# Optimization experiments

Measured on AMD Instinct MI355X. Metric: run time of the kernel, lower is better.

The kernel has to match this reference:

```python
import jax, jax.numpy as jnp
import numpy as np

B, A, L, D, IN = 4096, 11, 8, 256, 4
HID = 64  # mlp_dim in MS_HGNN modules
LINE = 64  # line_embedding output dim


def setup_inputs() -> dict:
    key = jax.random.key(0)
    ks = jax.random.split(key, 17)
    s = 0.02
    f = jnp.float32
    return {
        "inputs": jax.random.normal(ks[0], (B * A, L, IN), f),
        "W_in": jax.random.normal(ks[1], (IN, D), f) * s,
        "b_in": jnp.zeros((D,), f),
        "W_pos": jax.random.normal(ks[2], (2 * D, D), f) * s,
        "b_pos": jnp.zeros((D,), f),
        "W_fc2": jax.random.normal(ks[3], (L * D, D), f) * s,
        "b_fc2": jnp.zeros((D,), f),
        "W_fc3": jax.random.normal(ks[4], (D + A, D), f) * s,
        "b_fc3": jnp.zeros((D,), f),
        "Wh1": jax.random.normal(ks[5], (D, HID), f) * s,
        "We1": jax.random.normal(ks[6], (2 * HID, HID), f) * s,
        "Wn1": jax.random.normal(ks[7], (HID, D), f) * s,
        "Wh2": jax.random.normal(ks[8], (D, HID), f) * s,
        "We2": jax.random.normal(ks[9], (2 * HID, HID), f) * s,
        "Wn2": jax.random.normal(ks[10], (HID, D), f) * s,
        "W_line": jax.random.normal(ks[11], (D, LINE), f) * s,
        "batch_size": B,
        "agent_num": A,
    }


def _nmp(xf, Wh, We, Wn, w=None):
    # one round of neural message passing over the (hyper)graph of agents
    h = jax.nn.relu(xf @ Wh)  # [B, A, HID]
    b, a, hd = h.shape
    hi = jnp.broadcast_to(h[:, :, None, :], (b, a, a, hd))
    hj = jnp.broadcast_to(h[:, None, :, :], (b, a, a, hd))
    e = jax.nn.relu(jnp.concatenate([hi, hj], -1) @ We)  # [B, A, A, HID]
    if w is None:
        agg = e.mean(axis=2)
    else:
        agg = (w[..., None] * e).sum(axis=2) / (w.sum(axis=2)[..., None] + 1e-6)
    return agg @ Wn  # [B, A, D]


def reference(inputs, W_in, b_in, W_pos, b_pos, W_fc2, b_fc2, W_fc3, b_fc3,
              Wh1, We1, Wn1, Wh2, We2, Wn2, W_line, batch_size, agent_num):
    d = W_in.shape[1]
    length = inputs.shape[1]
    # input_fc
    tf_in = inputs @ W_in + b_in  # [B*A, L, D]
    # positional encoding (sin/cos interleaved), concat + fc (dropout in eval)
    pos = jnp.arange(length, dtype=tf_in.dtype)[:, None]
    div = jnp.exp(jnp.arange(0, d, 2, dtype=tf_in.dtype) * (-np.log(10000.0) / d))
    ang = pos * div  # [L, D/2]
    pe = jnp.stack([jnp.sin(ang), jnp.cos(ang)], -1).reshape(length, d)
    x = jnp.concatenate([tf_in, jnp.broadcast_to(pe, tf_in.shape)], -1) @ W_pos + b_pos
    # flatten time, input_fc2
    x = x.reshape(batch_size, agent_num, length * d)
    ftraj = x @ W_fc2 + b_fc2  # [B, A, D]
    # add_category (identity one-hot per agent) + input_fc3
    eye = jnp.broadcast_to(jnp.eye(agent_num, dtype=ftraj.dtype),
                           (batch_size, agent_num, agent_num))
    ftraj = jnp.concatenate([ftraj, eye], -1) @ W_fc3 + b_fc3
    # cosine-similarity correlation + per-scene adaptive thresholding
    q = ftraj / jnp.linalg.norm(ftraj, axis=2, keepdims=True)
    corr = jnp.einsum('bad,bcd->bac', q, q)
    a = corr.min(axis=(1, 2), keepdims=True)
    thr = jnp.where(a < 0.4, 0.4,
                    jnp.where((a > 0.4) & (a < 0.6), a + 0.1, a + 0.03))
    corr = jnp.where(corr < thr, jnp.zeros_like(corr), corr)
    adj = (corr > 0).astype(ftraj.dtype)  # binarized dynamic grouping mask
    # ordinary fully-connected interaction
    ftraj_inter = _nmp(ftraj, Wh1, We1, Wn1)
    # group-masked hyper interaction + line embedding
    hyp = _nmp(ftraj, Wh2, We2, Wn2, adj)
    feat_one = hyp @ W_line  # [B, A, LINE]
    out = jnp.concatenate([ftraj, ftraj_inter, feat_one], -1)
    return out.reshape(batch_size * agent_num, -1)
```

## Files before the change

### kernel.cpp

```cpp
#include <hip/hip_runtime.h>

#define TPB 256
#define TPM 192

constexpr int B_ = 4096, A_ = 11;
constexpr int R_ = B_ * A_;

constexpr int M_O     = 0;
constexpr int M2_O    = 8192;
constexpr int WC_O    = 16384;
constexpr int XB_O    = 17408;
constexpr int CB_O    = 19456;
constexpr int B2_O    = 19712;
constexpr int WN2L_O  = 22528;
constexpr int MH1_O   = 26624;
constexpr int BH1_O   = 28672;
constexpr int MH2_O   = 29376;
constexpr int BH2_O   = 31424;
constexpr int WFA1_O  = 32768;
constexpr int WFA2_O  = 49152;
constexpr int BEYE1_O = 65536;
constexpr int BEYE2_O = 66240;
constexpr int BB1_O   = 66944;
constexpr int BB2_O   = 67008;
constexpr int AG1_O   = 67584;
constexpr int SZ_RH   = R_ * 64;
constexpr int AG2_O   = AG1_O + SZ_RH;


__global__ __launch_bounds__(TPB) void k_preA(const float* __restrict__ Win,
                                              const float* __restrict__ bin,
                                              const float* __restrict__ Wpos,
                                              const float* __restrict__ bpos,
                                              const float* __restrict__ Wn2,
                                              const float* __restrict__ Wline,
                                              const float* __restrict__ Wfc3,
                                              const float* __restrict__ bfc3,
                                              const float* __restrict__ Wh1,
                                              const float* __restrict__ Wh2,
                                              float* __restrict__ ws) {
    __shared__ float red[8 * 33];
    const int t = threadIdx.x, o8 = t & 31, ks = t >> 5;
    const int bx = blockIdx.x;
    float p = 0.f;
    float base_add = 0.f;
    int out_idx = -1;
    if (bx < 64) {
        int o = bx * 32 + o8, l = o >> 8, j = o & 255;
        const float c0 = -logf(10000.f) / 256.f;
        for (int d = ks * 64; d < ks * 64 + 64; ++d) {
            float a;
            if (d < 256) a = bin[d];
            else {
                int dd = d - 256;
                float freq = expf((float)(dd & ~1) * c0);
                float ang = (float)l * freq;
                a = (dd & 1) ? cosf(ang) : sinf(ang);
            }
            p += a * Wpos[d * 256 + j];
        }
        out_idx = XB_O + o; base_add = bpos[j];
    } else if (bx < 192) {
        int o = (bx - 64) * 32 + o8, k = o >> 6, c = o & 63;
        #pragma unroll 8
        for (int d = ks * 32; d < ks * 32 + 32; ++d) p += Wn2[k * 256 + d] * Wline[d * 64 + c];
        out_idx = WN2L_O + o;
    } else if (bx < 704) {
        int o = (bx - 192) * 32 + o8, e = o >> 6, c = o & 63;
        #pragma unroll 8
        for (int d = ks * 32; d < ks * 32 + 32; ++d) p += Wfc3[e * 256 + d] * Wh1[d * 64 + c];
        out_idx = WFA1_O + o;
    } else if (bx < 1216) {
        int o = (bx - 704) * 32 + o8, e = o >> 6, c = o & 63;
        #pragma unroll 8
        for (int d = ks * 32; d < ks * 32 + 32; ++d) p += Wfc3[e * 256 + d] * Wh2[d * 64 + c];
        out_idx = WFA2_O + o;
    } else if (bx < 1238) {
        int o = (bx - 1216) * 32 + o8, a = o >> 6, c = o & 63;
        #pragma unroll 8
        for (int d = ks * 32; d < ks * 32 + 32; ++d) p += Wfc3[(256 + a) * 256 + d] * Wh1[d * 64 + c];
        out_idx = BEYE1_O + o;
    } else if (bx < 1260) {
        int o = (bx - 1238) * 32 + o8, a = o >> 6, c = o & 63;
        #pragma unroll 8
        for (int d = ks * 32; d < ks * 32 + 32; ++d) p += Wfc3[(256 + a) * 256 + d] * Wh2[d * 64 + c];
        out_idx = BEYE2_O + o;
    } else if (bx < 1262) {
        int c = (bx - 1260) * 32 + o8;
        #pragma unroll 8
        for (int d = ks * 32; d < ks * 32 + 32; ++d) p += bfc3[d] * Wh1[d * 64 + c];
        out_idx = BB1_O + c;
    } else if (bx < 1264) {
        int c = (bx - 1262) * 32 + o8;
        #pragma unroll 8
        for (int d = ks * 32; d < ks * 32 + 32; ++d) p += bfc3[d] * Wh2[d * 64 + c];
        out_idx = BB2_O + c;
    } else {
        int o = (bx - 1264) * 32 + o8, i = o >> 8, j = o & 255;
        #pragma unroll 8
        for (int d = ks * 32; d < ks * 32 + 32; ++d) p += Win[i * 256 + d] * Wpos[d * 256 + j];
        out_idx = WC_O + o;
    }
    red[ks * 33 + o8] = p;
    __shared__ float baseS[32];
    if (ks == 0) baseS[o8] = base_add;
    __syncthreads();
    if (t < 32) {
        float s = baseS[t];
        #pragma unroll
        for (int m = 0; m < 8; ++m) s += red[m * 33 + t];
        ws[out_idx - o8 + t] = s;
    }
}

__global__ __launch_bounds__(TPB) void k_preC(const float* __restrict__ Wfc2,
                                              const float* __restrict__ bfc2,
                                              float* __restrict__ ws) {
    __shared__ float red[8 * 33];
    const int t = threadIdx.x, o8 = t & 31, ks = t >> 5;
    const int bx = blockIdx.x;
    if (bx < 256) {
        int o = bx * 32 + o8, k = o >> 8, j = o & 255;
        int l = k >> 2, i = k & 3;
        const float* Ar = ws + WC_O + i * 256;
        const float* Br = Wfc2 + l * 65536 + j;
        float p = 0.f;
        #pragma unroll 8
        for (int d = ks * 32; d < ks * 32 + 32; ++d) p += Ar[d] * Br[d * 256];
        red[ks * 33 + o8] = p;
        __syncthreads();
        if (t < 32) {
            float s = 0.f;
            #pragma unroll
            for (int m = 0; m < 8; ++m) s += red[m * 33 + t];
            ws[M_O + bx * 32 + t] = s;
        }
    } else {
        int j = (bx - 256) * 32 + o8;
        const float* Ar = ws + XB_O;
        float p = 0.f;
        #pragma unroll 4
        for (int dk = ks * 256; dk < ks * 256 + 256; ++dk) p += Ar[dk] * Wfc2[dk * 256 + j];
        red[ks * 33 + o8] = p;
        __syncthreads();
        if (t < 32) {
            int jj = (bx - 256) * 32 + t;
            float s = bfc2[jj];
            #pragma unroll
            for (int m = 0; m < 8; ++m) s += red[m * 33 + t];
            ws[CB_O + jj] = s;
        }
    }
}

__global__ __launch_bounds__(TPB) void k_preD(const float* __restrict__ Wfc3,
                                              const float* __restrict__ bfc3,
                                              float* __restrict__ ws) {
    __shared__ float red[8 * 33];
    const int t = threadIdx.x, o8 = t & 31, ks = t >> 5;
    const int bx = blockIdx.x;
    float p = 0.f;
    int out_base = -1;
    int oo32 = 0;
    if (bx < 256) {
        int o = bx * 32 + o8, k = o >> 8, j = o & 255;
        const float* Ar = ws + M_O + k * 256;
        #pragma unroll 8
        for (int d = ks * 32; d < ks * 32 + 32; ++d) p += Ar[d] * Wfc3[d * 256 + j];
        out_base = M2_O; oo32 = bx * 32;
    } else if (bx < 344) {
        int o = (bx - 256) * 32 + o8, j = o & 255;
        const float* Ar = ws + CB_O;
        #pragma unroll 8
        for (int d = ks * 32; d < ks * 32 + 32; ++d) p += Ar[d] * Wfc3[d * 256 + j];
        out_base = B2_O; oo32 = (bx - 256) * 32;
    } else if (bx < 408) {
        int o = (bx - 344) * 32 + o8, k = o >> 6, c = o & 63;
        const float* Ar = ws + M_O + k * 256;
        const float* Br = ws + WFA1_O;
        #pragma unroll 8
        for (int d = ks * 32; d < ks * 32 + 32; ++d) p += Ar[d] * Br[d * 64 + c];
        out_base = MH1_O; oo32 = (bx - 344) * 32;
    } else if (bx < 472) {
        int o = (bx - 408) * 32 + o8, k = o >> 6, c = o & 63;
        const float* Ar = ws + M_O + k * 256;
        const float* Br = ws + WFA2_O;
        #pragma unroll 8
        for (int d = ks * 32; d < ks * 32 + 32; ++d) p += Ar[d] * Br[d * 64 + c];
        out_base = MH2_O; oo32 = (bx - 408) * 32;
    } else if (bx < 494) {
        int o = (bx - 472) * 32 + o8, c = o & 63;
        const float* Ar = ws + CB_O;
        const float* Br = ws + WFA1_O;
        #pragma unroll 8
        for (int d = ks * 32; d < ks * 32 + 32; ++d) p += Ar[d] * Br[d * 64 + c];
        out_base = BH1_O; oo32 = (bx - 472) * 32;
    } else {
        int o = (bx - 494) * 32 + o8, c = o & 63;
        const float* Ar = ws + CB_O;
        const float* Br = ws + WFA2_O;
        #pragma unroll 8
        for (int d = ks * 32; d < ks * 32 + 32; ++d) p += Ar[d] * Br[d * 64 + c];
        out_base = BH2_O; oo32 = (bx - 494) * 32;
    }
    red[ks * 33 + o8] = p;
    __syncthreads();
    if (t < 32) {
        int oo = oo32 + t;
        float s;
        if (out_base == B2_O) {
            int aa = oo >> 8, jj = oo & 255;
            s = bfc3[jj] + Wfc3[(256 + aa) * 256 + jj];
        } else if (out_base == BH1_O) {
            int aa = oo >> 6, cc = oo & 63;
            s = ws[BB1_O + cc] + ws[BEYE1_O + aa * 64 + cc];
        } else if (out_base == BH2_O) {
            int aa = oo >> 6, cc = oo & 63;
            s = ws[BB2_O + cc] + ws[BEYE2_O + aa * 64 + cc];
        } else s = 0.f;
        #pragma unroll
        for (int m = 0; m < 8; ++m) s += red[m * 33 + t];
        ws[out_base + oo] = s;
    }
}


__global__ __launch_bounds__(TPM) void k_main(const float* __restrict__ in,
                                              const float* __restrict__ We1g,
                                              const float* __restrict__ We2g,
                                              float* ws,
                                              float* out) {
    __shared__ float inS[22 * 36];
    __shared__ float buf[22 * 68];
    __shared__ float Bs[2048];
    __shared__ float dcS[242];
    __shared__ float thrS[2];
    const int t = threadIdx.x;
    const int rg = t >> 4, cg = t & 15;
    const int r0 = rg * 2, c0 = cg * 4;
    const int rowBlk = blockIdx.x * 22;
    const bool act = rg < 11;

    float4 pf0, pf1, pf2;
    auto pfLoad = [&](const float4* lo, const float4* hi) {
        pf0 = lo[t];
        pf1 = (t < 64) ? lo[t + 192] : hi[t - 64];
        if (t < 128) pf2 = hi[t + 128];
    };
    auto pfStore = [&]() {
        float4* d = (float4*)Bs;
        d[t] = pf0; d[t + 192] = pf1;
        if (t < 128) d[t + 384] = pf2;
    };

    pfLoad((const float4*)(ws + M2_O), (const float4*)(ws + M2_O) + 256);
    for (int o = t; o < 176; o += TPM) {
        int row = o >> 3, c4 = o & 7;
        *(float4*)&inS[row * 36 + c4 * 4] =
            *(const float4*)&in[(size_t)(rowBlk + row) * 32 + c4 * 4];
    }
    __syncthreads();

    float acc[2][16];
    #pragma unroll
    for (int r = 0; r < 2; ++r)
        #pragma unroll
        for (int c = 0; c < 16; ++c) acc[r][c] = 0.f;
    for (int kh = 0; kh < 4; ++kh) {
        pfStore();
        if (kh < 3) pfLoad((const float4*)(ws + M2_O) + (kh + 1) * 512,
                           (const float4*)(ws + M2_O) + (kh + 1) * 512 + 256);
        else        pfLoad((const float4*)(ws + MH1_O), (const float4*)(ws + MH1_O) + 256);
        __syncthreads();
        if (act) {
            #pragma unroll
            for (int kq = 0; kq < 2; ++kq) {
                float av[2][4];
                #pragma unroll
                for (int r = 0; r < 2; ++r) {
                    float4 a4 = *(const float4*)&inS[(r0 + r) * 36 + kh * 8 + kq * 4];
                    av[r][0] = a4.x; av[r][1] = a4.y; av[r][2] = a4.z; av[r][3] = a4.w;
                }
                #pragma unroll
                for (int kk = 0; kk < 4; ++kk) {
                    float4 b[4];
                    #pragma unroll
                    for (int j = 0; j < 4; ++j)
                        b[j] = *(const float4*)&Bs[(kq * 4 + kk) * 256 + c0 + j * 64];
                    #pragma unroll
                    for (int r = 0; r < 2; ++r) {
                        float a = av[r][kk];
                        #pragma unroll
                        for (int j = 0; j < 4; ++j) {
                            acc[r][j * 4 + 0] += a * b[j].x;
                            acc[r][j * 4 + 1] += a * b[j].y;
                            acc[r][j * 4 + 2] += a * b[j].z;
                            acc[r][j * 4 + 3] += a * b[j].w;
                        }
                    }
                }
            }
        }
        __syncthreads();
    }
    if (act) {
        #pragma unroll
        for (int r = 0; r < 2; ++r) {
            int row = r0 + r, il = row % 11;
            size_t ob = (size_t)(rowBlk + row) * 576;
            #pragma unroll
            for (int j = 0; j < 4; ++j) {
                float4 b2 = *(const float4*)&ws[B2_O + il * 256 + c0 + j * 64];
                acc[r][j * 4 + 0] += b2.x; acc[r][j * 4 + 1] += b2.y;
                acc[r][j * 4 + 2] += b2.z; acc[r][j * 4 + 3] += b2.w;
                *(float4*)&out[ob + c0 + j * 64] =
                    make_float4(acc[r][j * 4 + 0], acc[r][j * 4 + 1],
                                acc[r][j * 4 + 2], acc[r][j * 4 + 3]);
            }
        }
    }

    bool has0 = false;
    int s0_ = 0, i0_ = 0, j0_ = 0;
    if (t < 132) {
        has0 = true; s0_ = t / 66; int p = t % 66; int i = 0;
        while (p >= 11 - i) { p -= 11 - i; ++i; }
        i0_ = i; j0_ = i + p;
    }
    float dacc0 = 0.f;
    #pragma unroll
    for (int sl = 0; sl < 4; ++sl) {
        if (act) {
            #pragma unroll
            for (int r = 0; r < 2; ++r)
                *(float4*)&buf[(r0 + r) * 68 + c0] =
                    make_float4(acc[r][sl * 4 + 0], acc[r][sl * 4 + 1],
                                acc[r][sl * 4 + 2], acc[r][sl * 4 + 3]);
        }
        __syncthreads();
        if (has0) {
            const float* ra = &buf[(s0_ * 11 + i0_) * 68];
            const float* rb = &buf[(s0_ * 11 + j0_) * 68];
            #pragma unroll
            for (int c = 0; c < 16; ++c) {
                float4 a = *(const float4*)&ra[c * 4];
                float4 b = *(const float4*)&rb[c * 4];
                dacc0 += a.x * b.x + a.y * b.y + a.z * b.z + a.w * b.w;
            }
        }
        __syncthreads();
    }
    if (has0) { dcS[s0_ * 121 + i0_ * 11 + j0_] = dacc0;
                dcS[s0_ * 121 + j0_ * 11 + i0_] = dacc0; }
    __syncthreads();

    {
        float cc0, cc1 = 0.f;
        {
            int idx = t; int si = idx / 121, p = idx % 121, i = p / 11, j = p % 11;
            cc0 = dcS[idx] * rsqrtf(dcS[si * 121 + i * 12] * dcS[si * 121 + j * 12]);
        }
        if (t + TPM < 242) {
            int idx = t + TPM; int si = idx / 121, p = idx % 121, i = p / 11, j = p % 11;
            cc1 = dcS[idx] * rsqrtf(dcS[si * 121 + i * 12] * dcS[si * 121 + j * 12]);
        }
        __syncthreads();
        dcS[t] = cc0;
        if (t + TPM < 242) dcS[t + TPM] = cc1;
    }
    __syncthreads();
    if (t < 2) {
        float mn = 3.0e38f;
        for (int p = 0; p < 121; ++p) mn = fminf(mn, dcS[t * 121 + p]);
        thrS[t] = (mn < 0.4f) ? 0.4f : ((mn > 0.4f && mn < 0.6f) ? mn + 0.1f : mn + 0.03f);
    }
    __syncthreads();

    for (int st = 0; st < 2; ++st) {
        const float* bh = ws + (st ? BH2_O : BH1_O);
        const float* We = st ? We2g : We1g;
        pfStore();
        pfLoad((const float4*)(We), (const float4*)(We + 4096));
        __syncthreads();
        float hh[2][4];
        #pragma unroll
        for (int r = 0; r < 2; ++r)
            #pragma unroll
            for (int c = 0; c < 4; ++c) hh[r][c] = 0.f;
        if (act) {
            #pragma unroll
            for (int kq = 0; kq < 8; ++kq) {
                float av[2][4];
                #pragma unroll
                for (int r = 0; r < 2; ++r) {
                    float4 a4 = *(const float4*)&inS[(r0 + r) * 36 + kq * 4];
                    av[r][0] = a4.x; av[r][1] = a4.y; av[r][2] = a4.z; av[r][3] = a4.w;
                }
                #pragma unroll
                for (int kk = 0; kk < 4; ++kk) {
                    float4 b = *(const float4*)&Bs[(kq * 4 + kk) * 64 + c0];
                    #pragma unroll
                    for (int r = 0; r < 2; ++r) {
                        float a = av[r][kk];
                        hh[r][0] += a * b.x; hh[r][1] += a * b.y;
                        hh[r][2] += a * b.z; hh[r][3] += a * b.w;
                    }
                }
            }
            #pragma unroll
            for (int r = 0; r < 2; ++r) {
                int il = (r0 + r) % 11;
                float4 b = *(const float4*)&bh[il * 64 + c0];
                *(float4*)&buf[(r0 + r) * 68 + c0] =
                    make_float4(fmaxf(hh[r][0] + b.x, 0.f), fmaxf(hh[r][1] + b.y, 0.f),
                                fmaxf(hh[r][2] + b.z, 0.f), fmaxf(hh[r][3] + b.w, 0.f));
            }
        }
        __syncthreads();
        float uu[2][4], vv[2][4];
        #pragma unroll
        for (int r = 0; r < 2; ++r)
            #pragma unroll
            for (int c = 0; c < 4; ++c) { uu[r][c] = 0.f; vv[r][c] = 0.f; }
        for (int kh = 0; kh < 4; ++kh) {
            pfStore();
            if (kh < 3)
                pfLoad((const float4*)(We + (kh + 1) * 1024),
                       (const float4*)(We + 4096 + (kh + 1) * 1024));
            else if (st == 0)
                pfLoad((const float4*)(ws + MH2_O), (const float4*)(ws + MH2_O) + 256);
            __syncthreads();
            if (act) {
                #pragma unroll
                for (int kq = 0; kq < 4; ++kq) {
                    float av[2][4];
                    #pragma unroll
                    for (int r = 0; r < 2; ++r) {
                        float4 a4 = *(const float4*)&buf[(r0 + r) * 68 + kh * 16 + kq * 4];
                        av[r][0] = a4.x; av[r][1] = a4.y; av[r][2] = a4.z; av[r][3] = a4.w;
                    }
                    #pragma unroll
                    for (int kk = 0; kk < 4; ++kk) {
                        float4 bu = *(const float4*)&Bs[(kq * 4 + kk) * 64 + c0];
                        float4 bv = *(const float4*)&Bs[1024 + (kq * 4 + kk) * 64 + c0];
                        #pragma unroll
                        for (int r = 0; r < 2; ++r) {
                            float a = av[r][kk];
                            uu[r][0] += a * bu.x; uu[r][1] += a * bu.y;
                            uu[r][2] += a * bu.z; uu[r][3] += a * bu.w;
                            vv[r][0] += a * bv.x; vv[r][1] += a * bv.y;
                            vv[r][2] += a * bv.z; vv[r][3] += a * bv.w;
                        }
                    }
                }
            }
            __syncthreads();
        }
        if (act) {
            #pragma unroll
            for (int r = 0; r < 2; ++r)
                *(float4*)&buf[(r0 + r) * 68 + c0] =
                    make_float4(vv[r][0], vv[r][1], vv[r][2], vv[r][3]);
        }
        __syncthreads();
        if (act) {
            float* ag = ws + (st ? AG2_O : AG1_O);
            #pragma unroll
            for (int r = 0; r < 2; ++r) {
                int row = r0 + r, s = row / 11, il = row - s * 11;
                float th = thrS[s];
                float t0 = 0.f, t1 = 0.f, t2 = 0.f, t3 = 0.f, cnt = 0.f;
                #pragma unroll
                for (int j = 0; j < 11; ++j) {
                    float4 vj = *(const float4*)&buf[(s * 11 + j) * 68 + c0];
                    if (st == 0) {
                        t0 += fmaxf(uu[r][0] + vj.x, 0.f);
                        t1 += fmaxf(uu[r][1] + vj.y, 0.f);
                        t2 += fmaxf(uu[r][2] + vj.z, 0.f);
                        t3 += fmaxf(uu[r][3] + vj.w, 0.f);
                    } else {
                        float adj = (dcS[s * 121 + il * 11 + j] >= th) ? 1.f : 0.f;
                        t0 += adj * fmaxf(uu[r][0] + vj.x, 0.f);
                        t1 += adj * fmaxf(uu[r][1] + vj.y, 0.f);
                        t2 += adj * fmaxf(uu[r][2] + vj.z, 0.f);
                        t3 += adj * fmaxf(uu[r][3] + vj.w, 0.f);
                        cnt += adj;
                    }
                }
                float inv = (st == 0) ? (1.f / 11.f) : (1.f / (cnt + 1e-6f));
                *(float4*)&ag[(size_t)(rowBlk + row) * 64 + c0] =
                    make_float4(t0 * inv, t1 * inv, t2 * inv, t3 * inv);
            }
        }
        __syncthreads();
    }
}


__global__ __launch_bounds__(TPB) void k_tail(const float* __restrict__ Wn1,
                                              const float* __restrict__ ws,
                                              float* __restrict__ out) {
    __shared__ float aS[32 * 68];
    __shared__ float Bs[2048];
    const int t = threadIdx.x;
    const int rowBase = blockIdx.x * 32;
    const int tg = t >> 4, tc = t & 15;
    const int r0 = tg * 2, c0 = tc * 4;

    {
        const float4* s1 = (const float4*)(ws + AG1_O + (size_t)rowBase * 64);
        #pragma unroll
        for (int o = t; o < 512; o += TPB) {
            int row = o >> 4, c4 = o & 15;
            *(float4*)&aS[row * 68 + c4 * 4] = s1[o];
        }
    }
    __syncthreads();

    {
        float acc[2][16];
        #pragma unroll
        for (int r = 0; r < 2; ++r)
            #pragma unroll
            for (int c = 0; c < 16; ++c) acc[r][c] = 0.f;
        for (int kh = 0; kh < 8; ++kh) {
            if (kh) __syncthreads();
            {
                const float4* src = (const float4*)(Wn1 + kh * 2048);
                float4* dst = (float4*)Bs;
                dst[t] = src[t];
                dst[t + 256] = src[t + 256];
            }
            __syncthreads();
            #pragma unroll
            for (int kq = 0; kq < 2; ++kq) {
                float av[2][4];
                #pragma unroll
                for (int r = 0; r < 2; ++r) {
                    float4 a4 = *(const float4*)&aS[(r0 + r) * 68 + kh * 8 + kq * 4];
                    av[r][0] = a4.x; av[r][1] = a4.y; av[r][2] = a4.z; av[r][3] = a4.w;
                }
                #pragma unroll
                for (int kk = 0; kk < 4; ++kk) {
                    float4 b[4];
                    #pragma unroll
                    for (int j = 0; j < 4; ++j)
                        b[j] = *(const float4*)&Bs[(kq * 4 + kk) * 256 + c0 + j * 64];
                    #pragma unroll
                    for (int r = 0; r < 2; ++r) {
                        float a = av[r][kk];
                        #pragma unroll
                        for (int j = 0; j < 4; ++j) {
                            acc[r][j * 4 + 0] += a * b[j].x;
                            acc[r][j * 4 + 1] += a * b[j].y;
                            acc[r][j * 4 + 2] += a * b[j].z;
                            acc[r][j * 4 + 3] += a * b[j].w;
                        }
                    }
                }
            }
        }
        #pragma unroll
        for (int r = 0; r < 2; ++r) {
            size_t ob = (size_t)(rowBase + r0 + r) * 576 + 256;
            #pragma unroll
            for (int j = 0; j < 4; ++j)
                *(float4*)&out[ob + c0 + j * 64] =
                    make_float4(acc[r][j * 4 + 0], acc[r][j * 4 + 1],
                                acc[r][j * 4 + 2], acc[r][j * 4 + 3]);
        }
    }

    __syncthreads();
    {
        const float4* s2 = (const float4*)(ws + AG2_O + (size_t)rowBase * 64);
        #pragma unroll
        for (int o = t; o < 512; o += TPB) {
            int row = o >> 4, c4 = o & 15;
            *(float4*)&aS[row * 68 + c4 * 4] = s2[o];
        }
    }
    {
        float fa[2][4];
        #pragma unroll
        for (int r = 0; r < 2; ++r)
            #pragma unroll
            for (int c = 0; c < 4; ++c) fa[r][c] = 0.f;
        for (int kh = 0; kh < 2; ++kh) {
            __syncthreads();
            {
                const float4* src = (const float4*)(ws + WN2L_O + kh * 2048);
                float4* dst = (float4*)Bs;
                dst[t] = src[t];
                dst[t + 256] = src[t + 256];
            }
            __syncthreads();
            #pragma unroll
            for (int kq = 0; kq < 8; ++kq) {
                float av[2][4];
                #pragma unroll
                for (int r = 0; r < 2; ++r) {
                    float4 a4 = *(const float4*)&aS[(r0 + r) * 68 + kh * 32 + kq * 4];
                    av[r][0] = a4.x; av[r][1] = a4.y; av[r][2] = a4.z; av[r][3] = a4.w;
                }
                #pragma unroll
                for (int kk = 0; kk < 4; ++kk) {
                    float4 b = *(const float4*)&Bs[(kq * 4 + kk) * 64 + c0];
                    #pragma unroll
                    for (int r = 0; r < 2; ++r) {
                        float a = av[r][kk];
                        fa[r][0] += a * b.x; fa[r][1] += a * b.y;
                        fa[r][2] += a * b.z; fa[r][3] += a * b.w;
                    }
                }
            }
        }
        #pragma unroll
        for (int r = 0; r < 2; ++r)
            *(float4*)&out[(size_t)(rowBase + r0 + r) * 576 + 512 + c0] =
                make_float4(fa[r][0], fa[r][1], fa[r][2], fa[r][3]);
    }
}

extern "C" void kernel_launch(void* const* d_in, const int* in_sizes, int n_in,
                              void* d_out, int out_size, void* d_ws, size_t ws_size,
                              hipStream_t stream) {
    (void)in_sizes; (void)n_in; (void)out_size; (void)ws_size;
    const float* in     = (const float*)d_in[0];
    const float* W_in   = (const float*)d_in[1];
    const float* b_in   = (const float*)d_in[2];
    const float* W_pos  = (const float*)d_in[3];
    const float* b_pos  = (const float*)d_in[4];
    const float* W_fc2  = (const float*)d_in[5];
    const float* b_fc2  = (const float*)d_in[6];
    const float* W_fc3  = (const float*)d_in[7];
    const float* b_fc3  = (const float*)d_in[8];
    const float* Wh1    = (const float*)d_in[9];
    const float* We1    = (const float*)d_in[10];
    const float* Wn1    = (const float*)d_in[11];
    const float* Wh2    = (const float*)d_in[12];
    const float* We2    = (const float*)d_in[13];
    const float* Wn2    = (const float*)d_in[14];
    const float* W_line = (const float*)d_in[15];
    float* out = (float*)d_out;
    float* ws  = (float*)d_ws;

    k_preA<<<1296, TPB, 0, stream>>>(W_in, b_in, W_pos, b_pos, Wn2, W_line,
                                     W_fc3, b_fc3, Wh1, Wh2, ws);
    k_preC<<<264, TPB, 0, stream>>>(W_fc2, b_fc2, ws);
    k_preD<<<516, TPB, 0, stream>>>(W_fc3, b_fc3, ws);
    k_main<<<R_ / 22, TPM, 0, stream>>>(in, We1, We2, ws, out);
    k_tail<<<R_ / 32, TPB, 0, stream>>>(Wn1, ws, out);
}
```

Measured before the change: 155.6 us.

## Fuse weight-folding prekernels and trade prefetch pipelining for occupancy in main kernels

Merges the two weight-folding kernels into one 43-block kernel, so each block computes a full folded row and chains it through the W_fc3 and hypergraph projections held in shared memory. In k_main it drops the register-held prefetch double buffer in favour of plain synchronous staging into shared memory, and splits the B-fragment loads into halves. It also adds a min-blocks hint of 8 to k_main and k_tail, all aimed at cutting register pressure and raising occupancy. A separate correlation buffer replaces one barrier. The risk is that the fused prekernel has very little parallelism, with long serial 2048-step strided global loops per thread, and that the main kernel loses load/compute overlap.

Result: slower. 240.5 us (+54.5%).

```diff
diff --git a/kernel.cpp b/kernel.cpp
--- a/kernel.cpp
+++ b/kernel.cpp
@@ -6,11 +6,9 @@
 constexpr int B_ = 4096, A_ = 11;
 constexpr int R_ = B_ * A_;
 
-constexpr int M_O     = 0;
 constexpr int M2_O    = 8192;
 constexpr int WC_O    = 16384;
 constexpr int XB_O    = 17408;
-constexpr int CB_O    = 19456;
 constexpr int B2_O    = 19712;
 constexpr int WN2L_O  = 22528;
 constexpr int MH1_O   = 26624;
@@ -113,127 +111,72 @@
     }
 }
 
-__global__ __launch_bounds__(TPB) void k_preC(const float* __restrict__ Wfc2,
-                                              const float* __restrict__ bfc2,
-                                              float* __restrict__ ws) {
-    __shared__ float red[8 * 33];
-    const int t = threadIdx.x, o8 = t & 31, ks = t >> 5;
+
+__global__ __launch_bounds__(TPB) void k_preCD(const float* __restrict__ Wfc2,
+                                               const float* __restrict__ bfc2,
+                                               const float* __restrict__ Wfc3,
+                                               const float* __restrict__ bfc3,
+                                               float* __restrict__ ws) {
+    __shared__ float rowS[256];
+    const int t = threadIdx.x;
     const int bx = blockIdx.x;
-    if (bx < 256) {
-        int o = bx * 32 + o8, k = o >> 8, j = o & 255;
-        int l = k >> 2, i = k & 3;
-        const float* Ar = ws + WC_O + i * 256;
-        const float* Br = Wfc2 + l * 65536 + j;
-        float p = 0.f;
-        #pragma unroll 8
-        for (int d = ks * 32; d < ks * 32 + 32; ++d) p += Ar[d] * Br[d * 256];
-        red[ks * 33 + o8] = p;
-        __syncthreads();
-        if (t < 32) {
-            float s = 0.f;
-            #pragma unroll
-            for (int m = 0; m < 8; ++m) s += red[m * 33 + t];
-            ws[M_O + bx * 32 + t] = s;
+    if (bx < 32) {
+        const int k = bx, i = k & 3, l = k >> 2;
+        const float* WcR = ws + WC_O + i * 256;
+        const float* Bcol = Wfc2 + l * 65536 + t;
+        float m = 0.f;
+        #pragma unroll 8
+        for (int d = 0; d < 256; ++d) m += WcR[d] * Bcol[d * 256];
+        rowS[t] = m;
+        __syncthreads();
+        float s = 0.f;
+        #pragma unroll 8
+        for (int d = 0; d < 256; ++d) s += rowS[d] * Wfc3[d * 256 + t];
+        ws[M2_O + k * 256 + t] = s;
+        if (t < 128) {
+            const int c = t & 63;
+            const bool one = t < 64;
+            const float* WF = ws + (one ? WFA1_O : WFA2_O);
+            float sh = 0.f;
+            #pragma unroll 8
+            for (int d = 0; d < 256; ++d) sh += rowS[d] * WF[d * 64 + c];
+            ws[(one ? MH1_O : MH2_O) + k * 64 + c] = sh;
         }
     } else {
-        int j = (bx - 256) * 32 + o8;
-        const float* Ar = ws + XB_O;
-        float p = 0.f;
-        #pragma unroll 4
-        for (int dk = ks * 256; dk < ks * 256 + 256; ++dk) p += Ar[dk] * Wfc2[dk * 256 + j];
-        red[ks * 33 + o8] = p;
-        __syncthreads();
-        if (t < 32) {
-            int jj = (bx - 256) * 32 + t;
-            float s = bfc2[jj];
-            #pragma unroll
-            for (int m = 0; m < 8; ++m) s += red[m * 33 + t];
-            ws[CB_O + jj] = s;
+        const int a = bx - 32;
+        float cbv = bfc2[t];
+        const float* xb = ws + XB_O;
+        #pragma unroll 8
+        for (int dk = 0; dk < 2048; ++dk) cbv += xb[dk] * Wfc2[dk * 256 + t];
+        rowS[t] = cbv;
+        __syncthreads();
+        float s = bfc3[t] + Wfc3[(256 + a) * 256 + t];
+        #pragma unroll 8
+        for (int d = 0; d < 256; ++d) s += rowS[d] * Wfc3[d * 256 + t];
+        ws[B2_O + a * 256 + t] = s;
+        if (t < 128) {
+            const int c = t & 63;
+            const bool one = t < 64;
+            const float* WF = ws + (one ? WFA1_O : WFA2_O);
+            float sh = ws[(one ? BB1_O : BB2_O) + c] + ws[(one ? BEYE1_O : BEYE2_O) + a * 64 + c];
+            #pragma unroll 8
+            for (int d = 0; d < 256; ++d) sh += rowS[d] * WF[d * 64 + c];
+            ws[(one ? BH1_O : BH2_O) + a * 64 + c] = sh;
         }
     }
 }
 
-__global__ __launch_bounds__(TPB) void k_preD(const float* __restrict__ Wfc3,
-                                              const float* __restrict__ bfc3,
-                                              float* __restrict__ ws) {
-    __shared__ float red[8 * 33];
-    const int t = threadIdx.x, o8 = t & 31, ks = t >> 5;
-    const int bx = blockIdx.x;
-    float p = 0.f;
-    int out_base = -1;
-    int oo32 = 0;
-    if (bx < 256) {
-        int o = bx * 32 + o8, k = o >> 8, j = o & 255;
-        const float* Ar = ws + M_O + k * 256;
-        #pragma unroll 8
-        for (int d = ks * 32; d < ks * 32 + 32; ++d) p += Ar[d] * Wfc3[d * 256 + j];
-        out_base = M2_O; oo32 = bx * 32;
-    } else if (bx < 344) {
-        int o = (bx - 256) * 32 + o8, j = o & 255;
-        const float* Ar = ws + CB_O;
-        #pragma unroll 8
-        for (int d = ks * 32; d < ks * 32 + 32; ++d) p += Ar[d] * Wfc3[d * 256 + j];
-        out_base = B2_O; oo32 = (bx - 256) * 32;
-    } else if (bx < 408) {
-        int o = (bx - 344) * 32 + o8, k = o >> 6, c = o & 63;
-        const float* Ar = ws + M_O + k * 256;
-        const float* Br = ws + WFA1_O;
-        #pragma unroll 8
-        for (int d = ks * 32; d < ks * 32 + 32; ++d) p += Ar[d] * Br[d * 64 + c];
-        out_base = MH1_O; oo32 = (bx - 344) * 32;
-    } else if (bx < 472) {
-        int o = (bx - 408) * 32 + o8, k = o >> 6, c = o & 63;
-        const float* Ar = ws + M_O + k * 256;
-        const float* Br = ws + WFA2_O;
-        #pragma unroll 8
-        for (int d = ks * 32; d < ks * 32 + 32; ++d) p += Ar[d] * Br[d * 64 + c];
-        out_base = MH2_O; oo32 = (bx - 408) * 32;
-    } else if (bx < 494) {
-        int o = (bx - 472) * 32 + o8, c = o & 63;
-        const float* Ar = ws + CB_O;
-        const float* Br = ws + WFA1_O;
-        #pragma unroll 8
-        for (int d = ks * 32; d < ks * 32 + 32; ++d) p += Ar[d] * Br[d * 64 + c];
-        out_base = BH1_O; oo32 = (bx - 472) * 32;
-    } else {
-        int o = (bx - 494) * 32 + o8, c = o & 63;
-        const float* Ar = ws + CB_O;
-        const float* Br = ws + WFA2_O;
-        #pragma unroll 8
-        for (int d = ks * 32; d < ks * 32 + 32; ++d) p += Ar[d] * Br[d * 64 + c];
-        out_base = BH2_O; oo32 = (bx - 494) * 32;
-    }
-    red[ks * 33 + o8] = p;
-    __syncthreads();
-    if (t < 32) {
-        int oo = oo32 + t;
-        float s;
-        if (out_base == B2_O) {
-            int aa = oo >> 8, jj = oo & 255;
-            s = bfc3[jj] + Wfc3[(256 + aa) * 256 + jj];
-        } else if (out_base == BH1_O) {
-            int aa = oo >> 6, cc = oo & 63;
-            s = ws[BB1_O + cc] + ws[BEYE1_O + aa * 64 + cc];
-        } else if (out_base == BH2_O) {
-            int aa = oo >> 6, cc = oo & 63;
-            s = ws[BB2_O + cc] + ws[BEYE2_O + aa * 64 + cc];
-        } else s = 0.f;
-        #pragma unroll
-        for (int m = 0; m < 8; ++m) s += red[m * 33 + t];
-        ws[out_base + oo] = s;
-    }
-}
-
-
-__global__ __launch_bounds__(TPM) void k_main(const float* __restrict__ in,
-                                              const float* __restrict__ We1g,
-                                              const float* __restrict__ We2g,
-                                              float* ws,
-                                              float* out) {
+
+__global__ __launch_bounds__(TPM, 8) void k_main(const float* __restrict__ in,
+                                                 const float* __restrict__ We1g,
+                                                 const float* __restrict__ We2g,
+                                                 float* ws,
+                                                 float* out) {
     __shared__ float inS[22 * 36];
     __shared__ float buf[22 * 68];
     __shared__ float Bs[2048];
     __shared__ float dcS[242];
+    __shared__ float dcC[242];
     __shared__ float thrS[2];
     const int t = threadIdx.x;
     const int rg = t >> 4, cg = t & 15;
@@ -241,25 +184,19 @@
     const int rowBlk = blockIdx.x * 22;
     const bool act = rg < 11;
 
-    float4 pf0, pf1, pf2;
-    auto pfLoad = [&](const float4* lo, const float4* hi) {
-        pf0 = lo[t];
-        pf1 = (t < 64) ? lo[t + 192] : hi[t - 64];
-        if (t < 128) pf2 = hi[t + 128];
+    auto stageBs = [&](const float* src) {
+        const float4* s = (const float4*)src;
+        float4* d = (float4*)Bs;
+        d[t] = s[t];
+        d[t + 192] = s[t + 192];
+        if (t < 128) d[t + 384] = s[t + 384];
     };
-    auto pfStore = [&]() {
-        float4* d = (float4*)Bs;
-        d[t] = pf0; d[t + 192] = pf1;
-        if (t < 128) d[t + 384] = pf2;
-    };
-
-    pfLoad((const float4*)(ws + M2_O), (const float4*)(ws + M2_O) + 256);
+
     for (int o = t; o < 176; o += TPM) {
         int row = o >> 3, c4 = o & 7;
         *(float4*)&inS[row * 36 + c4 * 4] =
             *(const float4*)&in[(size_t)(rowBlk + row) * 32 + c4 * 4];
     }
-    __syncthreads();
 
     float acc[2][16];
     #pragma unroll
@@ -267,10 +204,8 @@
         #pragma unroll
         for (int c = 0; c < 16; ++c) acc[r][c] = 0.f;
     for (int kh = 0; kh < 4; ++kh) {
-        pfStore();
-        if (kh < 3) pfLoad((const float4*)(ws + M2_O) + (kh + 1) * 512,
-                           (const float4*)(ws + M2_O) + (kh + 1) * 512 + 256);
-        else        pfLoad((const float4*)(ws + MH1_O), (const float4*)(ws + MH1_O) + 256);
+        if (kh) __syncthreads();
+        stageBs(ws + M2_O + kh * 2048);
         __syncthreads();
         if (act) {
             #pragma unroll
@@ -283,19 +218,28 @@
                 }
                 #pragma unroll
                 for (int kk = 0; kk < 4; ++kk) {
-                    float4 b[4];
-                    #pragma unroll
-                    for (int j = 0; j < 4; ++j)
-                        b[j] = *(const float4*)&Bs[(kq * 4 + kk) * 256 + c0 + j * 64];
-                    #pragma unroll
-                    for (int r = 0; r < 2; ++r) {
-                        float a = av[r][kk];
+                    {
+                        float4 b0 = *(const float4*)&Bs[(kq * 4 + kk) * 256 + c0];
+                        float4 b1 = *(const float4*)&Bs[(kq * 4 + kk) * 256 + c0 + 64];
                         #pragma unroll
-                        for (int j = 0; j < 4; ++j) {
-                            acc[r][j * 4 + 0] += a * b[j].x;
-                            acc[r][j * 4 + 1] += a * b[j].y;
-                            acc[r][j * 4 + 2] += a * b[j].z;
-                            acc[r][j * 4 + 3] += a * b[j].w;
+                        for (int r = 0; r < 2; ++r) {
+                            float a = av[r][kk];
+                            acc[r][0] += a * b0.x; acc[r][1] += a * b0.y;
+                            acc[r][2] += a * b0.z; acc[r][3] += a * b0.w;
+                            acc[r][4] += a * b1.x; acc[r][5] += a * b1.y;
+                            acc[r][6] += a * b1.z; acc[r][7] += a * b1.w;
+                        }
+                    }
+                    {
+                        float4 b2 = *(const float4*)&Bs[(kq * 4 + kk) * 256 + c0 + 128];
+                        float4 b3 = *(const float4*)&Bs[(kq * 4 + kk) * 256 + c0 + 192];
+                        #pragma unroll
+                        for (int r = 0; r < 2; ++r) {
+                            float a = av[r][kk];
+                            acc[r][8]  += a * b2.x; acc[r][9]  += a * b2.y;
+                            acc[r][10] += a * b2.z; acc[r][11] += a * b2.w;
+                            acc[r][12] += a * b3.x; acc[r][13] += a * b3.y;
+                            acc[r][14] += a * b3.z; acc[r][15] += a * b3.w;
                         }
                     }
                 }
@@ -360,18 +304,18 @@
             int idx = t; int si = idx / 121, p = idx % 121, i = p / 11, j = p % 11;
             cc0 = dcS[idx] * rsqrtf(dcS[si * 121 + i * 12] * dcS[si * 121 + j * 12]);
         }
-        if (t + TPM < 242) {
+        const bool h2 = (t + TPM < 242);
+        if (h2) {
             int idx = t + TPM; int si = idx / 121, p = idx % 121, i = p / 11, j = p % 11;
             cc1 = dcS[idx] * rsqrtf(dcS[si * 121 + i * 12] * dcS[si * 121 + j * 12]);
         }
-        __syncthreads();
-        dcS[t] = cc0;
-        if (t + TPM < 242) dcS[t + TPM] = cc1;
+        dcC[t] = cc0;
+        if (h2) dcC[t + TPM] = cc1;
     }
     __syncthreads();
     if (t < 2) {
         float mn = 3.0e38f;
-        for (int p = 0; p < 121; ++p) mn = fminf(mn, dcS[t * 121 + p]);
+        for (int p = 0; p < 121; ++p) mn = fminf(mn, dcC[t * 121 + p]);
         thrS[t] = (mn < 0.4f) ? 0.4f : ((mn > 0.4f && mn < 0.6f) ? mn + 0.1f : mn + 0.03f);
     }
     __syncthreads();
@@ -379,8 +323,7 @@
     for (int st = 0; st < 2; ++st) {
         const float* bh = ws + (st ? BH2_O : BH1_O);
         const float* We = st ? We2g : We1g;
-        pfStore();
-        pfLoad((const float4*)(We), (const float4*)(We + 4096));
+        stageBs(ws + (st ? MH2_O : MH1_O));
         __syncthreads();
         float hh[2][4];
         #pragma unroll
@@ -423,12 +366,13 @@
             #pragma unroll
             for (int c = 0; c < 4; ++c) { uu[r][c] = 0.f; vv[r][c] = 0.f; }
         for (int kh = 0; kh < 4; ++kh) {
-            pfStore();
-            if (kh < 3)
-                pfLoad((const float4*)(We + (kh + 1) * 1024),
-                       (const float4*)(We + 4096 + (kh + 1) * 1024));
-            else if (st == 0)
-                pfLoad((const float4*)(ws + MH2_O), (const float4*)(ws + MH2_O) + 256);
+            if (kh) __syncthreads();
+            {
+                const float4* s0 = (const float4*)(We + kh * 1024);
+                const float4* s1 = (const float4*)(We + 4096 + kh * 1024);
+                float4* d = (float4*)Bs;
+                for (int o = t; o < 256; o += TPM) { d[o] = s0[o]; d[256 + o] = s1[o]; }
+            }
             __syncthreads();
             if (act) {
                 #pragma unroll
@@ -454,8 +398,8 @@
                     }
                 }
             }
-            __syncthreads();
-        }
+        }
+        __syncthreads();
         if (act) {
             #pragma unroll
             for (int r = 0; r < 2; ++r)
@@ -479,7 +423,7 @@
                         t2 += fmaxf(uu[r][2] + vj.z, 0.f);
                         t3 += fmaxf(uu[r][3] + vj.w, 0.f);
                     } else {
-                        float adj = (dcS[s * 121 + il * 11 + j] >= th) ? 1.f : 0.f;
+                        float adj = (dcC[s * 121 + il * 11 + j] >= th) ? 1.f : 0.f;
                         t0 += adj * fmaxf(uu[r][0] + vj.x, 0.f);
                         t1 += adj * fmaxf(uu[r][1] + vj.y, 0.f);
                         t2 += adj * fmaxf(uu[r][2] + vj.z, 0.f);
@@ -497,9 +441,9 @@
 }
 
 
-__global__ __launch_bounds__(TPB) void k_tail(const float* __restrict__ Wn1,
-                                              const float* __restrict__ ws,
-                                              float* __restrict__ out) {
+__global__ __launch_bounds__(TPB, 8) void k_tail(const float* __restrict__ Wn1,
+                                                 const float* __restrict__ ws,
+                                                 float* __restrict__ out) {
     __shared__ float aS[32 * 68];
     __shared__ float Bs[2048];
     const int t = threadIdx.x;
@@ -542,19 +486,28 @@
                 }
                 #pragma unroll
                 for (int kk = 0; kk < 4; ++kk) {
-                    float4 b[4];
-                    #pragma unroll
-                    for (int j = 0; j < 4; ++j)
-                        b[j] = *(const float4*)&Bs[(kq * 4 + kk) * 256 + c0 + j * 64];
-                    #pragma unroll
-                    for (int r = 0; r < 2; ++r) {
-                        float a = av[r][kk];
+                    {
+                        float4 b0 = *(const float4*)&Bs[(kq * 4 + kk) * 256 + c0];
+                        float4 b1 = *(const float4*)&Bs[(kq * 4 + kk) * 256 + c0 + 64];
                         #pragma unroll
-                        for (int j = 0; j < 4; ++j) {
-                            acc[r][j * 4 + 0] += a * b[j].x;
-                            acc[r][j * 4 + 1] += a * b[j].y;
-                            acc[r][j * 4 + 2] += a * b[j].z;
-                            acc[r][j * 4 + 3] += a * b[j].w;
+                        for (int r = 0; r < 2; ++r) {
+                            float a = av[r][kk];
+                            acc[r][0] += a * b0.x; acc[r][1] += a * b0.y;
+                            acc[r][2] += a * b0.z; acc[r][3] += a * b0.w;
+                            acc[r][4] += a * b1.x; acc[r][5] += a * b1.y;
+                            acc[r][6] += a * b1.z; acc[r][7] += a * b1.w;
+                        }
+                    }
+                    {
+                        float4 b2 = *(const float4*)&Bs[(kq * 4 + kk) * 256 + c0 + 128];
+                        float4 b3 = *(const float4*)&Bs[(kq * 4 + kk) * 256 + c0 + 192];
+                        #pragma unroll
+                        for (int r = 0; r < 2; ++r) {
+                            float a = av[r][kk];
+                            acc[r][8]  += a * b2.x; acc[r][9]  += a * b2.y;
+                            acc[r][10] += a * b2.z; acc[r][11] += a * b2.w;
+                            acc[r][12] += a * b3.x; acc[r][13] += a * b3.y;
+                            acc[r][14] += a * b3.z; acc[r][15] += a * b3.w;
                         }
                     }
                 }
@@ -647,8 +600,7 @@
 
     k_preA<<<1296, TPB, 0, stream>>>(W_in, b_in, W_pos, b_pos, Wn2, W_line,
                                      W_fc3, b_fc3, Wh1, Wh2, ws);
-    k_preC<<<264, TPB, 0, stream>>>(W_fc2, b_fc2, ws);
-    k_preD<<<516, TPB, 0, stream>>>(W_fc3, b_fc3, ws);
+    k_preCD<<<43, TPB, 0, stream>>>(W_fc2, b_fc2, W_fc3, b_fc3, ws);
     k_main<<<R_ / 22, TPM, 0, stream>>>(in, We1, We2, ws, out);
     k_tail<<<R_ / 32, TPB, 0, stream>>>(Wn1, ws, out);
 }
```
